# Optimization experiments

Hardware: AMD Instinct MI355X
Metric: run time of the kernel (lower is better)

Reference implementation:

```python
import jax, jax.numpy as jnp
import numpy as np

B, C, H, W = 1, 32, 128, 512
PAD = 40  # max disparity; output has PAD+1 planes


def setup_inputs() -> dict:
    key = jax.random.key(0)
    k1, k2 = jax.random.split(key)
    input_1 = jax.random.normal(k1, (B, C, H, W), dtype=jnp.float32)
    input_2 = jax.random.normal(k2, (B, C, H, W), dtype=jnp.float32)
    return {"input_1": input_1, "input_2": input_2, "pad_size": PAD}


def reference(input_1, input_2, pad_size):
    # input_1, input_2: [B, C, H, W]; pad_size: python int
    b, c, h, w = input_1.shape
    # left-pad input_2 along W with zeros (matches F.pad(pad=(pad_size,0,0,0)))
    padded = jnp.pad(input_2, ((0, 0), (0, 0), (0, 0), (pad_size, 0)))
    # torch loop: i = pad_size .. 0, appended in that order, so output plane d
    # uses slice starting at i = pad_size - d.
    d_idx = pad_size - jnp.arange(pad_size + 1)          # [D]
    gather_idx = d_idx[:, None] + jnp.arange(w)[None, :]  # [D, W]
    shifted = jnp.take(padded, gather_idx, axis=3)        # [B, C, H, D, W]
    shifted = jnp.moveaxis(shifted, 3, 2)                 # [B, C, D, H, W]
    # elementwise correlation cost volume
    return input_1[:, :, None, :, :] * shifted            # [B, C, D, H, W]
```

## Files before the change

### kernel.cpp

```cpp
#include <hip/hip_runtime.h>

constexpr int C = 32;
constexpr int H = 128;
constexpr int W = 512;
constexpr int PAD = 40;
constexpr int D = PAD + 1;
constexpr int W4 = W / 4;

__global__ __launch_bounds__(256)
void corr1d_kernel(const float* __restrict__ in1,
                   const float* __restrict__ in2,
                   float* __restrict__ out) {
    const int c  = blockIdx.y;
    const int h0 = blockIdx.x * 2;
    const int t  = threadIdx.x;
    const int r  = t >> 7;
    const int w4 = t & (W4 - 1);
    const int h  = h0 + r;

    __shared__ float4 s2[2][W4];

    const float4* in1v = (const float4*)in1;
    const float4* in2v = (const float4*)in2;
    const int rowIdx = (c * H + h) * W4;

    const float4 a = in1v[rowIdx + w4];
    s2[r][w4] = in2v[rowIdx + w4];
    __syncthreads();

    float4* outv = (float4*)out;
    const int obase = (c * D * H + h) * W4 + w4;

    const float4 zero4 = make_float4(0.f, 0.f, 0.f, 0.f);

    #pragma unroll
    for (int d = 0; d <= PAD; ++d) {
        const int q  = d >> 2;
        const int rr = d & 3;
        const int i0 = w4 - q;

        const float4 cur  = (i0     >= 0) ? s2[r][i0]     : zero4;
        const float4 prev = (i0 - 1 >= 0) ? s2[r][i0 - 1] : zero4;

        float b0, b1, b2, b3;
        switch (rr) {
            case 0:  b0 = cur.x;  b1 = cur.y;  b2 = cur.z;  b3 = cur.w; break;
            case 1:  b0 = prev.w; b1 = cur.x;  b2 = cur.y;  b3 = cur.z; break;
            case 2:  b0 = prev.z; b1 = prev.w; b2 = cur.x;  b3 = cur.y; break;
            default: b0 = prev.y; b1 = prev.z; b2 = prev.w; b3 = cur.x; break;
        }

        float4 res;
        res.x = a.x * b0;
        res.y = a.y * b1;
        res.z = a.z * b2;
        res.w = a.w * b3;

        outv[obase + d * H * W4] = res;
    }
}

extern "C" void kernel_launch(void* const* d_in, const int* in_sizes, int n_in,
                              void* d_out, int out_size, void* d_ws, size_t ws_size,
                              hipStream_t stream) {
    const float* in1 = (const float*)d_in[0];
    const float* in2 = (const float*)d_in[1];
    float* out = (float*)d_out;

    dim3 block(256);
    dim3 grid(H / 2, C);
    corr1d_kernel<<<grid, block, 0, stream>>>(in1, in2, out);
}
```

Before: 350.1 us.

## Parallelize over disparity per block with nontemporal streaming stores

Blocks now own one disparity plane and a 32-row band instead of two rows across all 41 planes. Each block writes one contiguous region of the output, reading its inputs straight from global memory, so shared memory and the barrier go away. Stores become nontemporal so the 107MB output bypasses cache. The cost is that inputs are re-read 41 times, though these reads should mostly hit L2 and the infinity cache.

```diff
diff --git a/kernel.cpp b/kernel.cpp
--- a/kernel.cpp
+++ b/kernel.cpp
@@ -6,57 +6,76 @@
 constexpr int PAD = 40;
 constexpr int D = PAD + 1;
 constexpr int W4 = W / 4;
+constexpr int RPB = 32;
+constexpr int QUADS = H / RPB;
+constexpr int ITERS = RPB / 2;
+
+typedef float f32x4 __attribute__((ext_vector_type(4)));
+
+template <int RR>
+__device__ __forceinline__
+void corr_loop(const float4* __restrict__ p1,
+               const float4* __restrict__ p2c,
+               const float4* __restrict__ p2p,
+               float4* po,
+               const bool curOk, const bool prevOk) {
+    const float4 zero4 = make_float4(0.f, 0.f, 0.f, 0.f);
+#pragma unroll 4
+    for (int i = 0; i < ITERS; ++i) {
+        float4 a   = *p1;
+        float4 cur = *p2c;
+        float4 prv = (RR == 0) ? zero4 : *p2p;
+        if (!curOk)             cur = zero4;
+        if (RR != 0 && !prevOk) prv = zero4;
+
+        float b0, b1, b2, b3;
+        if (RR == 0)      { b0 = cur.x; b1 = cur.y; b2 = cur.z; b3 = cur.w; }
+        else if (RR == 1) { b0 = prv.w; b1 = cur.x; b2 = cur.y; b3 = cur.z; }
+        else if (RR == 2) { b0 = prv.z; b1 = prv.w; b2 = cur.x; b3 = cur.y; }
+        else              { b0 = prv.y; b1 = prv.z; b2 = prv.w; b3 = cur.x; }
+
+        f32x4 res;
+        res.x = a.x * b0;
+        res.y = a.y * b1;
+        res.z = a.z * b2;
+        res.w = a.w * b3;
+
+        __builtin_nontemporal_store(res, (f32x4*)po);
+
+        p1 += 2 * W4; p2c += 2 * W4; p2p += 2 * W4; po += 2 * W4;
+    }
+}
 
 __global__ __launch_bounds__(256)
 void corr1d_kernel(const float* __restrict__ in1,
                    const float* __restrict__ in2,
                    float* __restrict__ out) {
-    const int c  = blockIdx.y;
-    const int h0 = blockIdx.x * 2;
+    const int c    = blockIdx.y;
+    const int d    = blockIdx.x >> 2;
+    const int quad = blockIdx.x & (QUADS - 1);
     const int t  = threadIdx.x;
     const int r  = t >> 7;
     const int w4 = t & (W4 - 1);
-    const int h  = h0 + r;
 
-    __shared__ float4 s2[2][W4];
+    const int q  = d >> 2;
+    const int i0 = w4 - q;
+    const bool curOk  = (i0 >= 0);
+    const bool prevOk = (i0 >= 1);
+    const int icur  = curOk  ? i0     : 0;
+    const int iprev = prevOk ? i0 - 1 : 0;
 
-    const float4* in1v = (const float4*)in1;
-    const float4* in2v = (const float4*)in2;
-    const int rowIdx = (c * H + h) * W4;
+    const int h = quad * RPB + r;
+    const int rowBase = (c * H + h) * W4;
+    const float4* p1  = (const float4*)in1 + rowBase + w4;
+    const float4* p2c = (const float4*)in2 + rowBase + icur;
+    const float4* p2p = (const float4*)in2 + rowBase + iprev;
+    float4*       po  = (float4*)out + ((c * D + d) * H + h) * W4 + w4;
 
-    const float4 a = in1v[rowIdx + w4];
-    s2[r][w4] = in2v[rowIdx + w4];
-    __syncthreads();
-
-    float4* outv = (float4*)out;
-    const int obase = (c * D * H + h) * W4 + w4;
-
-    const float4 zero4 = make_float4(0.f, 0.f, 0.f, 0.f);
-
-    #pragma unroll
-    for (int d = 0; d <= PAD; ++d) {
-        const int q  = d >> 2;
-        const int rr = d & 3;
-        const int i0 = w4 - q;
-
-        const float4 cur  = (i0     >= 0) ? s2[r][i0]     : zero4;
-        const float4 prev = (i0 - 1 >= 0) ? s2[r][i0 - 1] : zero4;
-
-        float b0, b1, b2, b3;
-        switch (rr) {
-            case 0:  b0 = cur.x;  b1 = cur.y;  b2 = cur.z;  b3 = cur.w; break;
-            case 1:  b0 = prev.w; b1 = cur.x;  b2 = cur.y;  b3 = cur.z; break;
-            case 2:  b0 = prev.z; b1 = prev.w; b2 = cur.x;  b3 = cur.y; break;
-            default: b0 = prev.y; b1 = prev.z; b2 = prev.w; b3 = cur.x; break;
-        }
-
-        float4 res;
-        res.x = a.x * b0;
-        res.y = a.y * b1;
-        res.z = a.z * b2;
-        res.w = a.w * b3;
-
-        outv[obase + d * H * W4] = res;
+    switch (d & 3) {
+        case 0:  corr_loop<0>(p1, p2c, p2p, po, curOk, prevOk); break;
+        case 1:  corr_loop<1>(p1, p2c, p2p, po, curOk, prevOk); break;
+        case 2:  corr_loop<2>(p1, p2c, p2p, po, curOk, prevOk); break;
+        default: corr_loop<3>(p1, p2c, p2p, po, curOk, prevOk); break;
     }
 }
 
@@ -68,6 +87,6 @@
     float* out = (float*)d_out;
 
     dim3 block(256);
-    dim3 grid(H / 2, C);
+    dim3 grid(D * QUADS, C);
     corr1d_kernel<<<grid, block, 0, stream>>>(in1, in2, out);
 }
```

Measured after the change: 390.4 us. +11.5%, slower.

## Split disparities into groups and loop rows per block, dropping shared memory

Applied to the files above, without the earlier changes.

Blocks now each handle a group of about seven disparity planes over a 16-row chunk, instead of two rows across all 41 disparities. The shifted in2 vectors are loaded directly from global memory with per-lane bounds masks, which removes the shared-memory staging and the barrier. The intent is more store work per thread with better write locality and less synchronization. In exchange, in2 is re-read from global or cache once per disparity group, and there are fewer blocks in total.

```diff
diff --git a/kernel.cpp b/kernel.cpp
--- a/kernel.cpp
+++ b/kernel.cpp
@@ -6,57 +6,99 @@
 constexpr int PAD = 40;
 constexpr int D = PAD + 1;
 constexpr int W4 = W / 4;
+constexpr int ROWS = 16;
+constexpr int CHUNKS = H / ROWS;
+constexpr int NGROUPS = 6;
+
+template <int D0, int G>
+__device__ __forceinline__
+void corr_group(const float4* __restrict__ in1v,
+                const float4* __restrict__ in2v,
+                float4* __restrict__ outv,
+                const int c, const int chunk) {
+    constexpr int Q0  = D0 >> 2;
+    constexpr int RR0 = D0 & 3;
+
+    const int t  = threadIdx.x;
+    const int r  = t >> 7;
+    const int w4 = t & (W4 - 1);
+
+    const int I = w4 - Q0;
+    const bool ok0 = (I >= 0), ok1 = (I >= 1), ok2 = (I >= 2), ok3 = (I >= 3);
+    const int i0 = ok0 ? I     : 0;
+    const int i1 = ok1 ? I - 1 : 0;
+    const int i2 = ok2 ? I - 2 : 0;
+    const int i3 = ok3 ? I - 3 : 0;
+
+    const int h = chunk * ROWS + r;
+    const int rowBase = (c * H + h) * W4;
+
+    const float4* p1  = in1v + rowBase + w4;
+    const float4* pw0 = in2v + rowBase + i0;
+    const float4* pw1 = in2v + rowBase + i1;
+    const float4* pw2 = in2v + rowBase + i2;
+    const float4* pw3 = in2v + rowBase + i3;
+    float4*       po  = outv + ((c * D + D0) * H + h) * W4 + w4;
+
+    const float4 z4 = make_float4(0.f, 0.f, 0.f, 0.f);
+
+#pragma unroll
+    for (int s = 0; s < ROWS / 2; ++s) {
+        const float4 a  = *p1;
+        const float4 w0 = ok0 ? *pw0 : z4;
+        const float4 w1 = ok1 ? *pw1 : z4;
+        const float4 w2 = ok2 ? *pw2 : z4;
+        const float4 w3 = ok3 ? *pw3 : z4;
+
+#pragma unroll
+        for (int j = 0; j < G; ++j) {
+            const int SEL = RR0 + j;
+            const int qo  = SEL >> 2;
+            const int rj  = SEL & 3;
+
+            const float4 cur  = (qo == 0) ? w0 : ((qo == 1) ? w1 : w2);
+            const float4 prev = (qo == 0) ? w1 : ((qo == 1) ? w2 : w3);
+
+            float b0, b1, b2, b3;
+            if      (rj == 0) { b0 = cur.x;  b1 = cur.y;  b2 = cur.z;  b3 = cur.w; }
+            else if (rj == 1) { b0 = prev.w; b1 = cur.x;  b2 = cur.y;  b3 = cur.z; }
+            else if (rj == 2) { b0 = prev.z; b1 = prev.w; b2 = cur.x;  b3 = cur.y; }
+            else              { b0 = prev.y; b1 = prev.z; b2 = prev.w; b3 = cur.x; }
+
+            float4 res;
+            res.x = a.x * b0;
+            res.y = a.y * b1;
+            res.z = a.z * b2;
+            res.w = a.w * b3;
+
+            po[j * H * W4] = res;
+        }
+
+        p1  += 2 * W4;
+        pw0 += 2 * W4;  pw1 += 2 * W4;  pw2 += 2 * W4;  pw3 += 2 * W4;
+        po  += 2 * W4;
+    }
+}
 
 __global__ __launch_bounds__(256)
 void corr1d_kernel(const float* __restrict__ in1,
                    const float* __restrict__ in2,
                    float* __restrict__ out) {
-    const int c  = blockIdx.y;
-    const int h0 = blockIdx.x * 2;
-    const int t  = threadIdx.x;
-    const int r  = t >> 7;
-    const int w4 = t & (W4 - 1);
-    const int h  = h0 + r;
-
-    __shared__ float4 s2[2][W4];
+    const int c     = blockIdx.y;
+    const int g     = blockIdx.x >> 3;
+    const int chunk = blockIdx.x & (CHUNKS - 1);
 
     const float4* in1v = (const float4*)in1;
     const float4* in2v = (const float4*)in2;
-    const int rowIdx = (c * H + h) * W4;
+    float4*       outv = (float4*)out;
 
-    const float4 a = in1v[rowIdx + w4];
-    s2[r][w4] = in2v[rowIdx + w4];
-    __syncthreads();
-
-    float4* outv = (float4*)out;
-    const int obase = (c * D * H + h) * W4 + w4;
-
-    const float4 zero4 = make_float4(0.f, 0.f, 0.f, 0.f);
-
-    #pragma unroll
-    for (int d = 0; d <= PAD; ++d) {
-        const int q  = d >> 2;
-        const int rr = d & 3;
-        const int i0 = w4 - q;
-
-        const float4 cur  = (i0     >= 0) ? s2[r][i0]     : zero4;
-        const float4 prev = (i0 - 1 >= 0) ? s2[r][i0 - 1] : zero4;
-
-        float b0, b1, b2, b3;
-        switch (rr) {
-            case 0:  b0 = cur.x;  b1 = cur.y;  b2 = cur.z;  b3 = cur.w; break;
-            case 1:  b0 = prev.w; b1 = cur.x;  b2 = cur.y;  b3 = cur.z; break;
-            case 2:  b0 = prev.z; b1 = prev.w; b2 = cur.x;  b3 = cur.y; break;
-            default: b0 = prev.y; b1 = prev.z; b2 = prev.w; b3 = cur.x; break;
-        }
-
-        float4 res;
-        res.x = a.x * b0;
-        res.y = a.y * b1;
-        res.z = a.z * b2;
-        res.w = a.w * b3;
-
-        outv[obase + d * H * W4] = res;
+    switch (g) {
+        case 0:  corr_group< 0, 7>(in1v, in2v, outv, c, chunk); break;
+        case 1:  corr_group< 7, 7>(in1v, in2v, outv, c, chunk); break;
+        case 2:  corr_group<14, 7>(in1v, in2v, outv, c, chunk); break;
+        case 3:  corr_group<21, 7>(in1v, in2v, outv, c, chunk); break;
+        case 4:  corr_group<28, 7>(in1v, in2v, outv, c, chunk); break;
+        default: corr_group<35, 6>(in1v, in2v, outv, c, chunk); break;
     }
 }
 
@@ -68,6 +110,6 @@
     float* out = (float*)d_out;
 
     dim3 block(256);
-    dim3 grid(H / 2, C);
+    dim3 grid(NGROUPS * CHUNKS, C);
     corr1d_kernel<<<grid, block, 0, stream>>>(in1, in2, out);
 }
```

New measurement: 362.9 us. 1.04x slower.

## Remap blocks to per-disparity half-planes with XCD-aware channel swizzle

Applied to the files above, without the earlier changes.

Each block now writes one disparity plane for half of the rows of one channel, instead of all 41 planes for two rows. Inputs are read straight from global memory (no shared memory or barrier), and channels are spread across the 8 XCDs so that each channel's input rows stay within one XCD's L2. The shift pattern is resolved at compile time through a template. This makes every block's writes a contiguous streaming run. The cost is that each input is re-read 41 times, which relies on L2 hits.

```diff
diff --git a/kernel.cpp b/kernel.cpp
--- a/kernel.cpp
+++ b/kernel.cpp
@@ -6,49 +6,30 @@
 constexpr int PAD = 40;
 constexpr int D = PAD + 1;
 constexpr int W4 = W / 4;
+constexpr int HALF = H / 2;
+constexpr int NXCD = 8;
+constexpr int PER_C = D * 2;
+constexpr int NBLK = C * PER_C;
 
-__global__ __launch_bounds__(256)
-void corr1d_kernel(const float* __restrict__ in1,
-                   const float* __restrict__ in2,
-                   float* __restrict__ out) {
-    const int c  = blockIdx.y;
-    const int h0 = blockIdx.x * 2;
-    const int t  = threadIdx.x;
-    const int r  = t >> 7;
-    const int w4 = t & (W4 - 1);
-    const int h  = h0 + r;
-
-    __shared__ float4 s2[2][W4];
-
-    const float4* in1v = (const float4*)in1;
-    const float4* in2v = (const float4*)in2;
-    const int rowIdx = (c * H + h) * W4;
-
-    const float4 a = in1v[rowIdx + w4];
-    s2[r][w4] = in2v[rowIdx + w4];
-    __syncthreads();
-
-    float4* outv = (float4*)out;
-    const int obase = (c * D * H + h) * W4 + w4;
-
-    const float4 zero4 = make_float4(0.f, 0.f, 0.f, 0.f);
-
-    #pragma unroll
-    for (int d = 0; d <= PAD; ++d) {
-        const int q  = d >> 2;
-        const int rr = d & 3;
-        const int i0 = w4 - q;
-
-        const float4 cur  = (i0     >= 0) ? s2[r][i0]     : zero4;
-        const float4 prev = (i0 - 1 >= 0) ? s2[r][i0 - 1] : zero4;
+template <int RR>
+__device__ __forceinline__
+void half_plane(const float4* __restrict__ p1,
+                const float4* __restrict__ pc,
+                const float4* __restrict__ pp,
+                float4* __restrict__ po,
+                const bool okc, const bool okp) {
+    const float4 z4 = make_float4(0.f, 0.f, 0.f, 0.f);
+#pragma unroll 8
+    for (int it = 0; it < HALF / 2; ++it) {
+        const float4 a   = *p1;
+        const float4 cur = okc ? *pc : z4;
+        const float4 prv = (RR == 0) ? z4 : (okp ? *pp : z4);
 
         float b0, b1, b2, b3;
-        switch (rr) {
-            case 0:  b0 = cur.x;  b1 = cur.y;  b2 = cur.z;  b3 = cur.w; break;
-            case 1:  b0 = prev.w; b1 = cur.x;  b2 = cur.y;  b3 = cur.z; break;
-            case 2:  b0 = prev.z; b1 = prev.w; b2 = cur.x;  b3 = cur.y; break;
-            default: b0 = prev.y; b1 = prev.z; b2 = prev.w; b3 = cur.x; break;
-        }
+        if      (RR == 0) { b0 = cur.x; b1 = cur.y; b2 = cur.z; b3 = cur.w; }
+        else if (RR == 1) { b0 = prv.w; b1 = cur.x; b2 = cur.y; b3 = cur.z; }
+        else if (RR == 2) { b0 = prv.z; b1 = prv.w; b2 = cur.x; b3 = cur.y; }
+        else              { b0 = prv.y; b1 = prv.z; b2 = prv.w; b3 = cur.x; }
 
         float4 res;
         res.x = a.x * b0;
@@ -56,7 +37,49 @@
         res.z = a.z * b2;
         res.w = a.w * b3;
 
-        outv[obase + d * H * W4] = res;
+        *po = res;
+
+        p1 += 2 * W4; pc += 2 * W4; pp += 2 * W4; po += 2 * W4;
+    }
+}
+
+__global__ __launch_bounds__(256)
+void corr1d_kernel(const float* __restrict__ in1,
+                   const float* __restrict__ in2,
+                   float* __restrict__ out) {
+    const int bid = blockIdx.x;
+    const int xcd = bid & (NXCD - 1);
+    const int g   = bid >> 3;
+    const int cg  = g / PER_C;
+    const int rem = g - cg * PER_C;
+    const int d    = rem >> 1;
+    const int half = rem & 1;
+    const int c    = cg * NXCD + xcd;
+
+    const int t  = threadIdx.x;
+    const int r  = t >> 7;
+    const int w4 = t & (W4 - 1);
+
+    const int q  = d >> 2;
+    const int I  = w4 - q;
+    const bool okc = (I >= 0);
+    const bool okp = (I >= 1);
+    const int ic = okc ? I     : 0;
+    const int ip = okp ? I - 1 : 0;
+
+    const int h = half * HALF + r;
+    const int rowBase = (c * H + h) * W4;
+
+    const float4* p1 = (const float4*)in1 + rowBase + w4;
+    const float4* pc = (const float4*)in2 + rowBase + ic;
+    const float4* pp = (const float4*)in2 + rowBase + ip;
+    float4*       po = (float4*)out + ((c * D + d) * H + h) * W4 + w4;
+
+    switch (d & 3) {
+        case 0:  half_plane<0>(p1, pc, pp, po, okc, okp); break;
+        case 1:  half_plane<1>(p1, pc, pp, po, okc, okp); break;
+        case 2:  half_plane<2>(p1, pc, pp, po, okc, okp); break;
+        default: half_plane<3>(p1, pc, pp, po, okc, okp); break;
     }
 }
 
@@ -68,6 +91,6 @@
     float* out = (float*)d_out;
 
     dim3 block(256);
-    dim3 grid(H / 2, C);
+    dim3 grid(NBLK);
     corr1d_kernel<<<grid, block, 0, stream>>>(in1, in2, out);
 }
```

New measurement: 426.4 us. +21.8%, slower.
